# Optimization experiments

Hardware: AMD Instinct MI355X
Metric: run time of the kernel (lower is better)

Reference implementation:

```python
import jax, jax.numpy as jnp
import numpy as np


def _lstm_layer(x, W, U, b):
    """Keras-style LSTM (gate order i,f,c,o). x: (B,T,F). Returns (hs: (B,T,H), h_last: (B,H))."""
    B, T, F = x.shape
    H = U.shape[0]
    # Precompute input projections for all timesteps: (T, B, 4H)
    zx = jnp.einsum('btf,fk->tbk', x, W) + b

    def step(carry, zx_t):
        h, c = carry
        z = zx_t + h @ U  # (B, 4H)
        i, f, g, o = jnp.split(z, 4, axis=-1)
        i = jax.nn.sigmoid(i)
        f = jax.nn.sigmoid(f)
        g = jnp.tanh(g)
        o = jax.nn.sigmoid(o)
        c = f * c + i * g
        h = o * jnp.tanh(c)
        return (h, c), h

    h0 = jnp.zeros((B, H), dtype=x.dtype)
    c0 = jnp.zeros((B, H), dtype=x.dtype)
    (h_last, _), hs = jax.lax.scan(step, (h0, c0), zx)
    return jnp.transpose(hs, (1, 0, 2)), h_last


def setup_inputs() -> dict:
    key = jax.random.key(0)
    ks = jax.random.split(key, 8)
    B, T, F, H, L = 512, 128, 64, 1024, 1
    s = 0.05
    return {
        'x': jax.random.normal(ks[0], (B, T, F), dtype=jnp.float32),
        'W1': jax.random.normal(ks[1], (F, 4 * H), dtype=jnp.float32) * s,
        'U1': jax.random.normal(ks[2], (H, 4 * H), dtype=jnp.float32) * s,
        'b1': jnp.zeros((4 * H,), dtype=jnp.float32),
        'W2': jax.random.normal(ks[3], (H, 4 * H), dtype=jnp.float32) * s,
        'U2': jax.random.normal(ks[4], (H, 4 * H), dtype=jnp.float32) * s,
        'b2': jnp.zeros((4 * H,), dtype=jnp.float32),
        'Wd': jax.random.normal(ks[5], (H, L), dtype=jnp.float32) * s,
        'bd': jnp.zeros((L,), dtype=jnp.float32),
    }


def reference(x, W1, U1, b1, W2, U2, b2, Wd, bd):
    # Layer 1: return_sequences=True (dropout inactive at inference)
    h1_seq, _ = _lstm_layer(x, W1, U1, b1)
    # Layer 2: return_sequences=False -> last hidden state
    _, h2_last = _lstm_layer(h1_seq, W2, U2, b2)
    # Dense sigmoid head
    return jax.nn.sigmoid(h2_last @ Wd + bd)
```

## Files before the change

kernel.cpp:

```cpp
#include <hip/hip_runtime.h>
#include <hip/hip_bf16.h>
#include <cstdint>


typedef __attribute__((ext_vector_type(8))) _Float16 half8;
typedef __attribute__((ext_vector_type(4))) float    float4v;

__device__ __forceinline__ float sigf(float x) { return 1.0f / (1.0f + __expf(-x)); }
__device__ __forceinline__ float tanhfast(float x) { return 2.0f * sigf(2.0f * x) - 1.0f; }

static constexpr size_t HPS = 32ull * 32 * 512;

struct FragSet {
    half8 A[4][4];
    half8 B[4][4];
};

__global__ __launch_bounds__(256, 1) void fused_step(
    int s,
    const _Float16* __restrict__ xp,
    const _Float16* __restrict__ P1,
    const _Float16* __restrict__ P2,
    const float* __restrict__ b1, float* __restrict__ c1, _Float16* __restrict__ h1p,
    const float* __restrict__ b2, float* __restrict__ c2, _Float16* __restrict__ h2p)
{
    const int b    = blockIdx.x;
    const int role = (b >> 3) & 1;
    const int tile = ((b >> 4) << 3) | (b & 7);

    const _Float16 *As0, *As1, *Pk;
    const float* bias; float* cs; _Float16* hop;
    int KC0, KCB, KCT;
    if (role == 0) {
        const int t = s; if (t >= 128) return;
        As0 = xp + (size_t)t * 32768;  KC0 = 2;
        As1 = h1p + (size_t)(t & 1) * HPS;
        Pk = P1; KCB = 34; KCT = 34;
        bias = b1; cs = c1;
        hop = h1p + (size_t)(1 - (t & 1)) * HPS;
    } else {
        const int t = s - 1; if (t < 0) return;
        As0 = h1p + (size_t)(1 - (t & 1)) * HPS; KC0 = 32;
        As1 = h2p + (size_t)(t & 1) * HPS;
        Pk = P2; KCB = 64; KCT = 64;
        bias = b2; cs = c2;
        hop = h2p + (size_t)(1 - (t & 1)) * HPS;
    }

    const int tid = threadIdx.x;
    const int w   = tid >> 6;
    const int l   = tid & 63;
    const int q   = l >> 4;
    const int c16 = l & 15;
    const int mh  = w & 1;
    const int nh  = w >> 1;

    const int m0  = (tile >> 5) * 128;
    const int n0  = (tile & 31) * 32;
    const int mG0 = (m0 >> 4) + mh * 4;

    const size_t l8 = (size_t)l * 8;

    const _Float16* bp[4];
#pragma unroll
    for (int g = 0; g < 4; ++g)
        bp[g] = Pk + ((size_t)(g * 64 + (n0 >> 4) + nh) * KCB) * 512 + l8;

    float4v acc[4][4] = {};

    auto loadS = [&](int st, FragSet& S) {
#pragma unroll
        for (int kcl = 0; kcl < 4; ++kcl) {
            const int kc = st * 4 + kcl;
            const _Float16* ab; size_t astr;
            if (kc < KC0) { ab = As0 + (size_t)kc * 512;         astr = (size_t)KC0 * 512; }
            else          { ab = As1 + (size_t)(kc - KC0) * 512; astr = 32ull * 512; }
            ab += (size_t)mG0 * astr + l8;
#pragma unroll
            for (int ms = 0; ms < 4; ++ms)
                S.A[ms][kcl] = *(const half8*)(ab + (size_t)ms * astr);
#pragma unroll
            for (int g = 0; g < 4; ++g)
                S.B[kcl][g] = *(const half8*)(bp[g] + (size_t)kc * 512);
        }
    };
    auto computeS = [&](const FragSet& S) {
#pragma unroll
        for (int kcl = 0; kcl < 4; ++kcl)
#pragma unroll
            for (int g = 0; g < 4; ++g)
#pragma unroll
                for (int ms = 0; ms < 4; ++ms)
                    acc[g][ms] = __builtin_amdgcn_mfma_f32_16x16x32_f16(
                        S.A[ms][kcl], S.B[kcl][g], acc[g][ms], 0, 0, 0);
    };

    const int NS = KCT >> 2;
    FragSet S0, S1;
    loadS(0, S0);
    for (int st = 0; st + 2 <= NS; st += 2) {
        loadS(st + 1, S1);
        computeS(S0);
        if (st + 2 < NS) loadS(st + 2, S0);
        computeS(S1);
    }
    if (KCT & 3) {
        half8 At[4][2], Bt[2][4];
#pragma unroll
        for (int kcl = 0; kcl < 2; ++kcl) {
            const int kc = NS * 4 + kcl;
            const _Float16* ab = As1 + (size_t)(kc - KC0) * 512
                               + (size_t)mG0 * (32ull * 512) + l8;
#pragma unroll
            for (int ms = 0; ms < 4; ++ms)
                At[ms][kcl] = *(const half8*)(ab + (size_t)ms * (32ull * 512));
#pragma unroll
            for (int g = 0; g < 4; ++g)
                Bt[kcl][g] = *(const half8*)(bp[g] + (size_t)kc * 512);
        }
#pragma unroll
        for (int kcl = 0; kcl < 2; ++kcl)
#pragma unroll
            for (int g = 0; g < 4; ++g)
#pragma unroll
                for (int ms = 0; ms < 4; ++ms)
                    acc[g][ms] = __builtin_amdgcn_mfma_f32_16x16x32_f16(
                        At[ms][kcl], Bt[kcl][g], acc[g][ms], 0, 0, 0);
    }

    const int ng = n0 + nh * 16 + c16;
    const float bi  = bias[ng];
    const float bff = bias[1024 + ng];
    const float bg  = bias[2048 + ng];
    const float bo  = bias[3072 + ng];
    const int kcH   = n0 >> 5;
    const int laneW = (nh * 2 + (c16 >> 3)) << 4;
    const int jW    = c16 & 7;
#pragma unroll
    for (int ms = 0; ms < 4; ++ms) {
        const int mG = mG0 + ms;
        _Float16* hg = hop + ((size_t)(mG * 32 + kcH)) * 512 + (size_t)laneW * 8 + jW;
#pragma unroll
        for (int i = 0; i < 4; ++i) {
            const int m = m0 + mh * 64 + ms * 16 + q * 4 + i;
            const float zi = acc[0][ms][i] + bi;
            const float zf = acc[1][ms][i] + bff;
            const float zg = acc[2][ms][i] + bg;
            const float zo = acc[3][ms][i] + bo;
            const float ig = sigf(zi);
            const float fg = sigf(zf);
            const float gg = tanhfast(zg);
            const float og = sigf(zo);
            const size_t cidx = (size_t)m * 1024 + ng;
            const float cc = fg * cs[cidx] + ig * gg;
            cs[cidx] = cc;
            hg[(q * 4 + i) * 8] = (_Float16)(og * tanhfast(cc));
        }
    }
}

__global__ void pack_weights(const float* __restrict__ W, const float* __restrict__ U,
                             int KA, int KC, _Float16* __restrict__ out)
{
    const size_t e = (size_t)blockIdx.x * blockDim.x + threadIdx.x;
    const size_t total = (size_t)256 * KC * 512;
    if (e >= total) return;
    const int j    = (int)(e & 7);
    const int lane = (int)((e >> 3) & 63);
    const size_t g = e >> 9;
    const int kc  = (int)(g % KC);
    const int ntG = (int)(g / KC);
    const int col = ntG * 16 + (lane & 15);
    const int k   = kc * 32 + (lane >> 4) * 8 + j;
    const float v = (k < KA) ? W[(size_t)k * 4096 + col]
                             : U[(size_t)(k - KA) * 4096 + col];
    out[e] = (_Float16)v;
}

__global__ void pack_x(const float* __restrict__ x, _Float16* __restrict__ xp)
{
    const int e = blockIdx.x * blockDim.x + threadIdx.x;
    if (e >= 512 * 128 * 64) return;
    const int j  = e & 7;
    const int l  = (e >> 3) & 63;
    const int g  = e >> 9;
    const int kc = g & 1;
    const int tm = g >> 1;
    const int mG = tm & 31;
    const int t  = tm >> 5;
    const int m  = mG * 16 + (l & 15);
    const int f  = kc * 32 + (l >> 4) * 8 + j;
    xp[e] = (_Float16)x[((size_t)m * 128 + t) * 64 + f];
}

__global__ __launch_bounds__(64) void dense_head(const _Float16* __restrict__ h2p,
                                                 const float* __restrict__ Wd,
                                                 const float* __restrict__ bd,
                                                 float* __restrict__ out)
{
    const int mG = blockIdx.x;
    const int l  = threadIdx.x;
    float s = 0.0f;
    for (int kc = 0; kc < 32; ++kc) {
        half8 f = *(const half8*)(h2p + ((size_t)(mG * 32 + kc)) * 512 + (size_t)l * 8);
        const int kb = kc * 32 + (l >> 4) * 8;
#pragma unroll
        for (int j = 0; j < 8; ++j) s += (float)f[j] * Wd[kb + j];
    }
    s += __shfl_xor(s, 16);
    s += __shfl_xor(s, 32);
    if (l < 16) out[mG * 16 + l] = 1.0f / (1.0f + __expf(-(s + bd[0])));
}


extern "C" void kernel_launch(void* const* d_in, const int* in_sizes, int n_in,
                              void* d_out, int out_size, void* d_ws, size_t ws_size,
                              hipStream_t stream)
{
    const float* x  = (const float*)d_in[0];
    const float* W1 = (const float*)d_in[1];
    const float* U1 = (const float*)d_in[2];
    const float* b1 = (const float*)d_in[3];
    const float* W2 = (const float*)d_in[4];
    const float* U2 = (const float*)d_in[5];
    const float* b2 = (const float*)d_in[6];
    const float* Wd = (const float*)d_in[7];
    const float* bd = (const float*)d_in[8];
    float* out = (float*)d_out;

    char* ws = (char*)d_ws;
    size_t off = 0;
    auto alloc = [&](size_t bytes) {
        char* p = ws + off;
        off = (off + bytes + 255) & ~(size_t)255;
        return p;
    };
    _Float16* xp  = (_Float16*)alloc(512ull * 128 * 64 * 2);
    _Float16* P1  = (_Float16*)alloc(256ull * 34 * 512 * 2);
    _Float16* P2  = (_Float16*)alloc(256ull * 64 * 512 * 2);
    _Float16* h1p = (_Float16*)alloc(2ull * HPS * 2);
    _Float16* h2p = (_Float16*)alloc(2ull * HPS * 2);
    float*    c1  = (float*)alloc(512ull * 1024 * 4);
    float*    c2  = (float*)alloc(512ull * 1024 * 4);

    hipMemsetAsync(c1, 0, 512ull * 1024 * 4, stream);
    hipMemsetAsync(c2, 0, 512ull * 1024 * 4, stream);
    hipMemsetAsync(h1p, 0, HPS * 2, stream);
    hipMemsetAsync(h2p, 0, HPS * 2, stream);

    pack_x<<<(512 * 128 * 64 + 255) / 256, 256, 0, stream>>>(x, xp);
    pack_weights<<<(256 * 34 * 512 + 255) / 256, 256, 0, stream>>>(W1, U1, 64, 34, P1);
    pack_weights<<<(256 * 64 * 512 + 255) / 256, 256, 0, stream>>>(W2, U2, 1024, 64, P2);

    for (int s = 0; s <= 128; ++s) {
        fused_step<<<256, 256, 0, stream>>>(s, xp, P1, P2,
                                            b1, c1, h1p, b2, c2, h2p);
    }
    dense_head<<<32, 64, 0, stream>>>(h2p, Wd, bd, out);
}
```

Measured before the change: 3.484 ms.

## Split K across wave pairs and reduce partial gate sums through LDS

The waves that previously split the N dimension now split the K range in half. Each wave computes both 16-column N fragments over its half of K, and the partial accumulators are exchanged and summed through a shared-memory buffer after a block barrier. Each A fragment is now reused across two N fragments, which reduces redundant A loads per wave. The cost is twice as many accumulator registers, an LDS round-trip with a __syncthreads, and smaller per-iteration load batches in the double-buffered pipeline.

Measured after the change: 3.186 ms. 1.09x faster.

```diff
diff --git a/kernel.cpp b/kernel.cpp
--- a/kernel.cpp
+++ b/kernel.cpp
@@ -12,8 +12,8 @@
 static constexpr size_t HPS = 32ull * 32 * 512;
 
 struct FragSet {
-    half8 A[4][4];
-    half8 B[4][4];
+    half8 A[4];
+    half8 B[4][2];
 };
 
 __global__ __launch_bounds__(256, 1) void fused_step(
@@ -53,7 +53,7 @@
     const int q   = l >> 4;
     const int c16 = l & 15;
     const int mh  = w & 1;
-    const int nh  = w >> 1;
+    const int kp  = w >> 1;
 
     const int m0  = (tile >> 5) * 128;
     const int n0  = (tile & 31) * 32;
@@ -61,80 +61,92 @@
 
     const size_t l8 = (size_t)l * 8;
 
-    const _Float16* bp[4];
+    const _Float16* bp[4][2];
 #pragma unroll
     for (int g = 0; g < 4; ++g)
-        bp[g] = Pk + ((size_t)(g * 64 + (n0 >> 4) + nh) * KCB) * 512 + l8;
-
-    float4v acc[4][4] = {};
-
-    auto loadS = [&](int st, FragSet& S) {
-#pragma unroll
-        for (int kcl = 0; kcl < 4; ++kcl) {
-            const int kc = st * 4 + kcl;
-            const _Float16* ab; size_t astr;
-            if (kc < KC0) { ab = As0 + (size_t)kc * 512;         astr = (size_t)KC0 * 512; }
-            else          { ab = As1 + (size_t)(kc - KC0) * 512; astr = 32ull * 512; }
-            ab += (size_t)mG0 * astr + l8;
-#pragma unroll
-            for (int ms = 0; ms < 4; ++ms)
-                S.A[ms][kcl] = *(const half8*)(ab + (size_t)ms * astr);
-#pragma unroll
-            for (int g = 0; g < 4; ++g)
-                S.B[kcl][g] = *(const half8*)(bp[g] + (size_t)kc * 512);
-        }
+#pragma unroll
+        for (int nf = 0; nf < 2; ++nf)
+            bp[g][nf] = Pk + ((size_t)(g * 64 + (n0 >> 4) + nf) * KCB) * 512 + l8;
+
+    float4v acc[4][4][2] = {};
+
+    auto loadS = [&](int kc, FragSet& S) {
+        const _Float16* ab; size_t astr;
+        if (kc < KC0) { ab = As0 + (size_t)kc * 512;         astr = (size_t)KC0 * 512; }
+        else          { ab = As1 + (size_t)(kc - KC0) * 512; astr = 32ull * 512; }
+        ab += (size_t)mG0 * astr + l8;
+#pragma unroll
+        for (int ms = 0; ms < 4; ++ms)
+            S.A[ms] = *(const half8*)(ab + (size_t)ms * astr);
+#pragma unroll
+        for (int g = 0; g < 4; ++g)
+#pragma unroll
+            for (int nf = 0; nf < 2; ++nf)
+                S.B[g][nf] = *(const half8*)(bp[g][nf] + (size_t)kc * 512);
     };
     auto computeS = [&](const FragSet& S) {
 #pragma unroll
-        for (int kcl = 0; kcl < 4; ++kcl)
-#pragma unroll
-            for (int g = 0; g < 4; ++g)
-#pragma unroll
-                for (int ms = 0; ms < 4; ++ms)
-                    acc[g][ms] = __builtin_amdgcn_mfma_f32_16x16x32_f16(
-                        S.A[ms][kcl], S.B[kcl][g], acc[g][ms], 0, 0, 0);
+        for (int g = 0; g < 4; ++g)
+#pragma unroll
+            for (int ms = 0; ms < 4; ++ms)
+#pragma unroll
+                for (int nf = 0; nf < 2; ++nf)
+                    acc[g][ms][nf] = __builtin_amdgcn_mfma_f32_16x16x32_f16(
+                        S.A[ms], S.B[g][nf], acc[g][ms][nf], 0, 0, 0);
     };
 
-    const int NS = KCT >> 2;
+    const int KCH = KCT >> 1;
+    const int kcS = kp ? KCH : 0;
+    const int kcE = kp ? KCT : KCH;
+
     FragSet S0, S1;
-    loadS(0, S0);
-    for (int st = 0; st + 2 <= NS; st += 2) {
-        loadS(st + 1, S1);
+    loadS(kcS, S0);
+    int kc = kcS;
+    for (; kc + 2 <= kcE; kc += 2) {
+        loadS(kc + 1, S1);
         computeS(S0);
-        if (st + 2 < NS) loadS(st + 2, S0);
+        if (kc + 2 < kcE) loadS(kc + 2, S0);
         computeS(S1);
     }
-    if (KCT & 3) {
-        half8 At[4][2], Bt[2][4];
-#pragma unroll
-        for (int kcl = 0; kcl < 2; ++kcl) {
-            const int kc = NS * 4 + kcl;
-            const _Float16* ab = As1 + (size_t)(kc - KC0) * 512
-                               + (size_t)mG0 * (32ull * 512) + l8;
-#pragma unroll
-            for (int ms = 0; ms < 4; ++ms)
-                At[ms][kcl] = *(const half8*)(ab + (size_t)ms * (32ull * 512));
-#pragma unroll
-            for (int g = 0; g < 4; ++g)
-                Bt[kcl][g] = *(const half8*)(bp[g] + (size_t)kc * 512);
-        }
-#pragma unroll
-        for (int kcl = 0; kcl < 2; ++kcl)
-#pragma unroll
-            for (int g = 0; g < 4; ++g)
-#pragma unroll
-                for (int ms = 0; ms < 4; ++ms)
-                    acc[g][ms] = __builtin_amdgcn_mfma_f32_16x16x32_f16(
-                        At[ms][kcl], Bt[kcl][g], acc[g][ms], 0, 0, 0);
-    }
-
-    const int ng = n0 + nh * 16 + c16;
+    if (kc < kcE) computeS(S0);
+
+    __shared__ float4v red[4][16][64];
+    if (kp == 0) {
+#pragma unroll
+        for (int g = 0; g < 4; ++g)
+#pragma unroll
+            for (int ms = 0; ms < 4; ++ms)
+                red[w][g * 4 + ms][l] = acc[g][ms][1];
+    } else {
+#pragma unroll
+        for (int g = 0; g < 4; ++g)
+#pragma unroll
+            for (int ms = 0; ms < 4; ++ms)
+                red[w][g * 4 + ms][l] = acc[g][ms][0];
+    }
+    __syncthreads();
+    float4v out[4][4];
+    if (kp == 0) {
+#pragma unroll
+        for (int g = 0; g < 4; ++g)
+#pragma unroll
+            for (int ms = 0; ms < 4; ++ms)
+                out[g][ms] = acc[g][ms][0] + red[w ^ 2][g * 4 + ms][l];
+    } else {
+#pragma unroll
+        for (int g = 0; g < 4; ++g)
+#pragma unroll
+            for (int ms = 0; ms < 4; ++ms)
+                out[g][ms] = acc[g][ms][1] + red[w ^ 2][g * 4 + ms][l];
+    }
+
+    const int ng = n0 + kp * 16 + c16;
     const float bi  = bias[ng];
     const float bff = bias[1024 + ng];
     const float bg  = bias[2048 + ng];
     const float bo  = bias[3072 + ng];
     const int kcH   = n0 >> 5;
-    const int laneW = (nh * 2 + (c16 >> 3)) << 4;
+    const int laneW = (kp * 2 + (c16 >> 3)) << 4;
     const int jW    = c16 & 7;
 #pragma unroll
     for (int ms = 0; ms < 4; ++ms) {
@@ -143,10 +155,10 @@
 #pragma unroll
         for (int i = 0; i < 4; ++i) {
             const int m = m0 + mh * 64 + ms * 16 + q * 4 + i;
-            const float zi = acc[0][ms][i] + bi;
-            const float zf = acc[1][ms][i] + bff;
-            const float zg = acc[2][ms][i] + bg;
-            const float zo = acc[3][ms][i] + bo;
+            const float zi = out[0][ms][i] + bi;
+            const float zf = out[1][ms][i] + bff;
+            const float zg = out[2][ms][i] + bg;
+            const float zo = out[3][ms][i] + bo;
             const float ig = sigf(zi);
             const float fg = sigf(zf);
             const float gg = tanhfast(zg);
```
